# Optimization experiments

Hardware: AMD Instinct MI355X
Metric: run time of the kernel (lower is better)

## Reference

```python
import jax, jax.numpy as jnp
import numpy as np

N = 100000      # nodes
E = 1600000     # edges (avg degree 16)
F_IN = 128      # node feature dim
F_OUT = 128     # GCN output dim


def setup_inputs() -> dict:
    key = jax.random.key(0)
    ks = jax.random.split(key, 11)
    s = 0.05  # weight scale to keep activations sane
    return {
        "x": jax.random.normal(ks[0], (N, F_IN), jnp.float32),
        "edge_index": jax.random.randint(ks[1], (2, E), 0, N, jnp.int32),
        "W": jax.random.normal(ks[2], (F_IN, F_OUT), jnp.float32) * s,
        "p": jax.random.normal(ks[3], (F_IN,), jnp.float32),
        "w_ih": jax.random.normal(ks[4], (3 * F_OUT, F_IN), jnp.float32) * s,
        "w_hh": jax.random.normal(ks[5], (3 * F_OUT, F_OUT), jnp.float32) * s,
        "b_ih": jax.random.normal(ks[6], (3 * F_OUT,), jnp.float32) * s,
        "b_hh": jax.random.normal(ks[7], (3 * F_OUT,), jnp.float32) * s,
        "conv_bias": jax.random.normal(ks[8], (F_OUT,), jnp.float32) * s,
        "lin_w": jax.random.normal(ks[9], (1, F_OUT), jnp.float32) * s,
        "lin_b": jax.random.normal(ks[10], (1,), jnp.float32) * s,
    }


def reference(x, edge_index, W, p, w_ih, w_hh, b_ih, b_hh, conv_bias, lin_w, lin_b):
    n_nodes = x.shape[0]
    k, H = W.shape  # k = F_IN rows, H = F_OUT hidden size

    # --- TopK summarize: pick k nodes, gate by tanh(score) -> X_tilde [k, F_IN]
    scores = x @ p / jnp.linalg.norm(p)
    top_vals, top_idx = jax.lax.top_k(scores, k)
    x_tilde = x[top_idx] * jnp.tanh(top_vals)[:, None]

    # --- one GRU step evolving W (hidden state = rows of W)
    gi = x_tilde @ w_ih.T + b_ih   # [k, 3H]
    gh = W @ w_hh.T + b_hh         # [k, 3H]
    r = jax.nn.sigmoid(gi[:, :H] + gh[:, :H])
    z = jax.nn.sigmoid(gi[:, H:2 * H] + gh[:, H:2 * H])
    n = jnp.tanh(gi[:, 2 * H:] + r * gh[:, 2 * H:])
    W_new = (1.0 - z) * n + z * W  # [F_IN, F_OUT]

    # --- GCN conv with fixed W: sym-normalized adjacency with self loops
    row, col = edge_index[0], edge_index[1]
    deg = jax.ops.segment_sum(jnp.ones_like(row, dtype=x.dtype), col,
                              num_segments=n_nodes) + 1.0  # +1 for self loop
    dinv = jax.lax.rsqrt(deg)
    xw = x @ W_new                                   # [N, F_OUT]
    coef = dinv[row] * dinv[col]                     # [E]
    agg = jax.ops.segment_sum(xw[row] * coef[:, None], col, num_segments=n_nodes)
    agg = agg + xw * (dinv * dinv)[:, None] + conv_bias  # self-loop term + bias

    # --- head: ReLU + Linear(F_OUT, 1)
    h = jax.nn.relu(agg)
    return h @ lin_w.T + lin_b  # [N, 1]
```

## Files before the change

kernel.cpp:

```cpp
#include <hip/hip_runtime.h>
#include <math.h>

#define N_NODES 100000
#define N_EDGES 1600000
#define F 128

#define BSH 8
#define NBUCK 391
#define BCAP 5120
#define PB_EDGES 2048
#define NB_PART 782
#define NB_SCORES 1563
#define NB_COLLECT 392

typedef unsigned int u32;
typedef unsigned short u16;
typedef __attribute__((ext_vector_type(8))) short short8;
typedef __attribute__((ext_vector_type(4))) float floatx4;
typedef __attribute__((ext_vector_type(2))) float f32x2;
typedef __attribute__((ext_vector_type(4))) u32 u32x4;


__device__ __forceinline__ u32 key_of(float s) {
    u32 u = __float_as_uint(s);
    return (u & 0x80000000u) ? ~u : (u | 0x80000000u);
}

__device__ __forceinline__ float wave_reduce(float v) {
    #pragma unroll
    for (int off = 32; off > 0; off >>= 1) v += __shfl_down(v, off, 64);
    return v;
}

__device__ __forceinline__ u16 f2bf(float f) {
    u32 u = __float_as_uint(f);
    u += 0x7fffu + ((u >> 16) & 1u);
    return (u16)(u >> 16);
}

__device__ __forceinline__ float bflo(u32 b) { return __uint_as_float(b << 16); }
__device__ __forceinline__ float bfhi(u32 b) { return __uint_as_float(b & 0xffff0000u); }

__device__ __forceinline__ void pk_acc(f32x2& acc, u32 u) {
    f32x2 v; v.x = bflo(u); v.y = bfhi(u);
    asm("v_pk_add_f32 %0, %1, %0" : "+v"(acc) : "v"(v));
}
__device__ __forceinline__ void pk_add2(f32x2& a, f32x2 b) {
    asm("v_pk_add_f32 %0, %1, %0" : "+v"(a) : "v"(b));
}


__global__ void k_front(const float* __restrict__ x, const float* __restrict__ p,
                        const int* __restrict__ ei, float* __restrict__ scores,
                        u32* __restrict__ hist16, u32* __restrict__ gcur,
                        u32* __restrict__ pairs, u32* __restrict__ xb) {
    if (blockIdx.x < NB_PART) {
        __shared__ u32 lh[NBUCK];
        __shared__ u32 lbase[NBUCK];
        int t = threadIdx.x;
        int e0 = blockIdx.x * PB_EDGES;
        int e1 = e0 + PB_EDGES; if (e1 > N_EDGES) e1 = N_EDGES;
        for (int i = t; i < NBUCK; i += 256) lh[i] = 0u;
        __syncthreads();
        for (int e = e0 + t; e < e1; e += 256)
            atomicAdd(&lh[((u32)ei[N_EDGES + e]) >> BSH], 1u);
        __syncthreads();
        for (int b = t; b < NBUCK; b += 256) {
            u32 c = lh[b];
            lbase[b] = c ? atomicAdd(&gcur[b], c) : 0u;
            lh[b] = 0u;
        }
        __syncthreads();
        for (int e = e0 + t; e < e1; e += 256) {
            u32 d = (u32)ei[N_EDGES + e];
            u32 b = d >> BSH;
            u32 pos = lbase[b] + atomicAdd(&lh[b], 1u);
            pairs[(size_t)b * BCAP + pos] = ((d & 255u) << 17) | (u32)ei[e];
        }
    } else {
        int sb = blockIdx.x - NB_PART;
        int wave = threadIdx.x >> 6;
        int lane = threadIdx.x & 63;
        int q = lane >> 4, sub = lane & 15;
        int nb0 = sb * 64 + wave * 16 + q;
        float4 p0 = *(const float4*)&p[sub * 8];
        float4 p1 = *(const float4*)&p[sub * 8 + 4];
        float4 v0[4], v1[4];
        if (nb0 + 12 < N_NODES) {
            #pragma unroll
            for (int r = 0; r < 4; r++) {
                const float* xr = &x[(size_t)(nb0 + r * 4) * F + sub * 8];
                v0[r] = *(const float4*)xr;
                v1[r] = *(const float4*)(xr + 4);
            }
        } else {
            #pragma unroll
            for (int r = 0; r < 4; r++) {
                int node = nb0 + r * 4;
                v0[r] = make_float4(0.f, 0.f, 0.f, 0.f);
                v1[r] = make_float4(0.f, 0.f, 0.f, 0.f);
                if (node < N_NODES) {
                    const float* xr = &x[(size_t)node * F + sub * 8];
                    v0[r] = *(const float4*)xr;
                    v1[r] = *(const float4*)(xr + 4);
                }
            }
        }
        #pragma unroll
        for (int r = 0; r < 4; r++) {
            int node = nb0 + r * 4;
            if (node >= N_NODES) continue;
            if (xb) {
                u32x4 pk;
                pk.x = (u32)f2bf(v0[r].x) | ((u32)f2bf(v0[r].y) << 16);
                pk.y = (u32)f2bf(v0[r].z) | ((u32)f2bf(v0[r].w) << 16);
                pk.z = (u32)f2bf(v1[r].x) | ((u32)f2bf(v1[r].y) << 16);
                pk.w = (u32)f2bf(v1[r].z) | ((u32)f2bf(v1[r].w) << 16);
                *(u32x4*)&xb[(size_t)node * 64 + sub * 4] = pk;
            }
            float d = v0[r].x * p0.x + v0[r].y * p0.y + v0[r].z * p0.z + v0[r].w * p0.w
                    + v1[r].x * p1.x + v1[r].y * p1.y + v1[r].z * p1.z + v1[r].w * p1.w;
            #pragma unroll
            for (int off = 1; off < 16; off <<= 1) d += __shfl_xor(d, off, 64);
            if (sub == 0) {
                scores[node] = d;
                atomicAdd(&hist16[key_of(d) >> 16], 1u);
            }
        }
    }
}


__global__ __launch_bounds__(1024) void k_scan16(const u32* __restrict__ hist16,
                                                 u32* __restrict__ state,
                                                 const u32* __restrict__ gcur,
                                                 u32* __restrict__ bbase) {
    __shared__ u32 a[1024];
    int t = threadIdx.x;
    if (blockIdx.x == 0) {
        const uint4* h4 = (const uint4*)hist16;
        u32 local = 0;
        #pragma unroll
        for (int i = 0; i < 16; i++) {
            uint4 v = h4[t * 16 + i];
            local += v.x + v.y + v.z + v.w;
        }
        a[t] = local;
        __syncthreads();
        for (int off = 1; off < 1024; off <<= 1) {
            u32 add = (t + off < 1024) ? a[t + off] : 0u;
            __syncthreads();
            a[t] += add;
            __syncthreads();
        }
        u32 S_above = (t == 1023) ? 0u : a[t + 1];
        if (S_above < 128u && a[t] >= 128u) {
            u32 cum = S_above;
            for (int v = t * 64 + 63; v >= t * 64; v--) {
                cum += hist16[v];
                if (cum >= 128u) { state[0] = (u32)v; break; }
            }
        }
    } else {
        u32 v = (t < NBUCK) ? gcur[t] : 0u;
        a[t] = v;
        __syncthreads();
        for (int off = 1; off < 1024; off <<= 1) {
            u32 add = (t >= off) ? a[t - off] : 0u;
            __syncthreads();
            a[t] += add;
            __syncthreads();
        }
        if (t < NBUCK) bbase[t] = a[t] - v;
    }
}


__global__ __launch_bounds__(256) void k_mid(const float* __restrict__ scores,
                                             u32* __restrict__ state,
                                             u32* __restrict__ cand,
                                             const u32* __restrict__ pairs,
                                             const u32* __restrict__ gcur,
                                             const u32* __restrict__ bbase,
                                             u32* __restrict__ offs,
                                             float* __restrict__ dinv,
                                             u32* __restrict__ ebuf) {
    if (blockIdx.x < NB_COLLECT) {
        u32 T = state[0] << 16;
        int i = blockIdx.x * 256 + threadIdx.x;
        if (i < N_NODES) {
            if (key_of(scores[i]) >= T) {
                u32 pos = atomicAdd(&state[2], 1u);
                if (pos < 2048u) cand[pos] = (u32)i;
            }
        }
    } else {
        __shared__ u32 h[256];
        __shared__ u32 sc[256];
        int b = blockIdx.x - NB_COLLECT, t = threadIdx.x;
        u32 base = bbase[b];
        u32 cnt  = gcur[b];
        const u32* seg = pairs + (size_t)b * BCAP;
        u32 lo = (u32)b << BSH;
        h[t] = 0u;
        __syncthreads();
        for (u32 i = t; i < cnt; i += 256)
            atomicAdd(&h[seg[i] >> 17], 1u);
        __syncthreads();
        sc[t] = h[t];
        __syncthreads();
        for (int off = 1; off < 256; off <<= 1) {
            u32 v = (t >= off) ? sc[t - off] : 0u;
            __syncthreads();
            sc[t] += v;
            __syncthreads();
        }
        int nn = N_NODES - (int)lo;
        if (t < nn) {
            u32 c = h[t];
            offs[lo + t] = base + (sc[t] - c);
            dinv[lo + t] = rsqrtf((float)c + 1.0f);
        }
        u32 excl = sc[t] - h[t];
        __syncthreads();
        sc[t] = excl;
        __syncthreads();
        for (u32 i = t; i < cnt; i += 256) {
            u32 pr = seg[i];
            u32 pos = base + atomicAdd(&sc[pr >> 17], 1u);
            ebuf[pos] = pr & 0x1ffffu;
        }
        if (b == 0 && t == 0) offs[N_NODES] = N_EDGES;
    }
}

__global__ void k_assemble16(const float* __restrict__ scores, const float* __restrict__ p,
                             const u32* __restrict__ state, const u32* __restrict__ cand,
                             u32* __restrict__ top_idx, float* __restrict__ gate) {
    __shared__ u32 ci[2048];
    __shared__ float csc[2048];
    __shared__ float s_inv;
    int t = threadIdx.x;
    if (t < 64) {
        float2 pv = *(const float2*)&p[t * 2];
        float d = pv.x * pv.x + pv.y * pv.y;
        d = wave_reduce(d);
        if (t == 0) s_inv = rsqrtf(d);
    }
    u32 nc = state[2]; if (nc > 2048u) nc = 2048u;
    for (u32 i = t; i < nc; i += 256) { u32 ix = cand[i]; ci[i] = ix; csc[i] = scores[ix]; }
    __syncthreads();
    for (u32 i = t; i < nc; i += 256) {
        u32 myk = key_of(csc[i]);
        u32 myi = ci[i];
        int rank = 0;
        for (u32 j = 0; j < nc; j++) {
            u32 ok = key_of(csc[j]);
            rank += (int)((ok > myk) || (ok == myk && ci[j] < myi));
        }
        if (rank < 128) {
            top_idx[rank] = myi;
            gate[rank] = tanhf(csc[i] * s_inv);
        }
    }
}


__global__ __launch_bounds__(256) void k_ggemm(const float* __restrict__ x,
                                               const float* __restrict__ W,
                                               const float* __restrict__ w_ih,
                                               const float* __restrict__ w_hh,
                                               const u32* __restrict__ top_idx,
                                               const float* __restrict__ gate,
                                               float* __restrict__ G) {
    __shared__ float As[32][128];
    __shared__ float Bs[64][131];
    int t = threadIdx.x;
    int k0 = blockIdx.x * 32;
    int by = blockIdx.y;
    int j0 = by * 64;
    bool is_gi = (by < 6);
    #pragma unroll
    for (int i = 0; i < 4; i++) {
        int l = t + i * 256;
        int row = l >> 5, c4 = l & 31;
        float4 v;
        if (is_gi) {
            u32 idx = top_idx[k0 + row];
            float gt = gate[k0 + row];
            v = *(const float4*)&x[(size_t)idx * F + c4 * 4];
            v.x *= gt; v.y *= gt; v.z *= gt; v.w *= gt;
        } else {
            v = *(const float4*)&W[(k0 + row) * F + c4 * 4];
        }
        *(float4*)&As[row][c4 * 4] = v;
    }
    const float* mat = is_gi ? w_ih : w_hh;
    int jbase = is_gi ? j0 : (j0 - 384);
    #pragma unroll
    for (int i = 0; i < 8; i++) {
        int l = t + i * 256;
        int row = l >> 5, c4 = l & 31;
        float4 v = *(const float4*)&mat[(jbase + row) * F + c4 * 4];
        Bs[row][c4 * 4 + 0] = v.x; Bs[row][c4 * 4 + 1] = v.y;
        Bs[row][c4 * 4 + 2] = v.z; Bs[row][c4 * 4 + 3] = v.w;
    }
    __syncthreads();
    int ty = t >> 5, tx = t & 31;
    float acc[4][2] = {};
    #pragma unroll 4
    for (int f = 0; f < 128; f++) {
        float b0 = Bs[tx * 2][f], b1 = Bs[tx * 2 + 1][f];
        #pragma unroll
        for (int i = 0; i < 4; i++) {
            float a = As[ty * 4 + i][f];
            acc[i][0] += a * b0;
            acc[i][1] += a * b1;
        }
    }
    #pragma unroll
    for (int i = 0; i < 4; i++) {
        int k = k0 + ty * 4 + i;
        G[(size_t)k * 768 + j0 + tx * 2 + 0] = acc[i][0];
        G[(size_t)k * 768 + j0 + tx * 2 + 1] = acc[i][1];
    }
}


__global__ void k_gate(const float* __restrict__ G, const float* __restrict__ W,
                       const float* __restrict__ b_ih, const float* __restrict__ b_hh,
                       float* __restrict__ Wnew, u16* __restrict__ Bfrag) {
    int idx = blockIdx.x * blockDim.x + threadIdx.x;
    int k = idx >> 7, h = idx & 127;
    const float* gk = &G[(size_t)k * 768];
    float gir = gk[h]       + b_ih[h];
    float giz = gk[128 + h] + b_ih[128 + h];
    float gin = gk[256 + h] + b_ih[256 + h];
    float ghr = gk[384 + h] + b_hh[h];
    float ghz = gk[512 + h] + b_hh[128 + h];
    float ghn = gk[640 + h] + b_hh[256 + h];
    float wv  = W[k * F + h];
    float rg = 1.0f / (1.0f + expf(-(gir + ghr)));
    float z  = 1.0f / (1.0f + expf(-(giz + ghz)));
    float n  = tanhf(gin + rg * ghn);
    float val = (1.0f - z) * n + z * wv;
    Wnew[k * F + h] = val;
    int nb = h >> 4, kc = k >> 5, q = (k >> 3) & 3, m = h & 15, jj = k & 7;
    Bfrag[(((nb * 4 + kc) * 64) + q * 16 + m) * 8 + jj] = f2bf(val);
}


__device__ __forceinline__ void gemm_core(u16* As, const u16* __restrict__ Bfrag,
                                          const float* __restrict__ dinv,
                                          u16* __restrict__ yw, int r0, int t) {
    int wv = t >> 6, lane = t & 63;
    int q = lane >> 4, m = lane & 15;
    floatx4 acc[8] = {};
    #pragma unroll
    for (int kc = 0; kc < 4; kc++) {
        short8 a = *(const short8*)&As[((wv * 4 + kc) * 64 + lane) * 8];
        #pragma unroll
        for (int nb = 0; nb < 8; nb++) {
            short8 bfr = *(const short8*)&Bfrag[((nb * 4 + kc) * 64 + lane) * 8];
            acc[nb] = __builtin_amdgcn_mfma_f32_16x16x32_bf16(a, bfr, acc[nb], 0, 0, 0);
        }
    }
    __syncthreads();

    float d[4];
    #pragma unroll
    for (int reg = 0; reg < 4; reg++) {
        int gr = r0 + wv * 16 + q * 4 + reg;
        d[reg] = (gr < N_NODES) ? dinv[gr] : 0.f;
    }
    #pragma unroll
    for (int nb = 0; nb < 8; nb++) {
        #pragma unroll
        for (int reg = 0; reg < 4; reg++) {
            int row = wv * 16 + q * 4 + reg;
            As[row * 132 + nb * 16 + m] = f2bf(acc[nb][reg] * d[reg]);
        }
    }
    __syncthreads();
    {
        int row = t >> 2, segi = t & 3;
        int gr = r0 + row;
        if (gr < N_NODES) {
            const uint2* src = (const uint2*)&As[row * 132 + segi * 32];
            uint2* dst = (uint2*)&yw[(size_t)gr * F + segi * 32];
            #pragma unroll
            for (int i = 0; i < 8; i++) dst[i] = src[i];
        }
    }
}

__global__ __launch_bounds__(256) void k_gemm(const float* __restrict__ x,
                                              const u16* __restrict__ Bfrag,
                                              const float* __restrict__ dinv,
                                              u16* __restrict__ yw) {
    __shared__ __align__(16) u16 As[8448];
    int t = threadIdx.x;
    int r0 = blockIdx.x * 64;
    #pragma unroll
    for (int i = 0; i < 8; i++) {
        int l = t + i * 256;
        int row = l >> 5, c4 = l & 31;
        int f0 = c4 * 4;
        float4 v = {0.f, 0.f, 0.f, 0.f};
        if (r0 + row < N_NODES) v = *(const float4*)&x[(size_t)(r0 + row) * F + f0];
        int widx = (((row >> 4) * 4 + (f0 >> 5)) * 64 + ((f0 >> 3) & 3) * 16 + (row & 15)) * 8
                   + (f0 & 7);
        ushort4 s4;
        s4.x = f2bf(v.x); s4.y = f2bf(v.y); s4.z = f2bf(v.z); s4.w = f2bf(v.w);
        *(ushort4*)&As[widx] = s4;
    }
    __syncthreads();
    gemm_core(As, Bfrag, dinv, yw, r0, t);
}

__global__ __launch_bounds__(256) void k_gemm_xb(const u32* __restrict__ xb,
                                                 const u16* __restrict__ Bfrag,
                                                 const float* __restrict__ dinv,
                                                 u16* __restrict__ yw) {
    __shared__ __align__(16) u16 As[8448];
    int t = threadIdx.x;
    int r0 = blockIdx.x * 64;
    #pragma unroll
    for (int i = 0; i < 4; i++) {
        int wdx = t + i * 256;
        int lane = wdx & 63, chunk = wdx >> 6;
        int kc = chunk & 3, rowhi = chunk >> 2;
        int q = lane >> 4, m = lane & 15;
        int row = rowhi * 16 + m;
        u32x4 v = {0u, 0u, 0u, 0u};
        if (r0 + row < N_NODES)
            v = *(const u32x4*)&xb[(size_t)(r0 + row) * 64 + kc * 16 + q * 4];
        *(u32x4*)&As[wdx * 8] = v;
    }
    __syncthreads();
    gemm_core(As, Bfrag, dinv, yw, r0, t);
}


#define EDGE_GROUP(J) {                                                      \
    u32 r = ebuf[(J) + q];                                                   \
    uint4 bb = *(const uint4*)&yw32[(size_t)r * 64 + sub * 4];               \
    pk_acc(a01, bb.x); pk_acc(a23, bb.y);                                    \
    pk_acc(a45, bb.z); pk_acc(a67, bb.w); }

#define BFLY(A) {                                                            \
    f32x2 tb;                                                                \
    tb.x = __shfl_xor(A.x, 16, 64); tb.y = __shfl_xor(A.y, 16, 64);          \
    pk_add2(A, tb);                                                          \
    tb.x = __shfl_xor(A.x, 32, 64); tb.y = __shfl_xor(A.y, 32, 64);          \
    pk_add2(A, tb); }

__global__ void k_gather(const u32* __restrict__ yw32, const u32* __restrict__ offs,
                         const u32* __restrict__ ebuf, const float* __restrict__ dinv,
                         const float* __restrict__ conv_bias, const float* __restrict__ lin_w,
                         const float* __restrict__ lin_b, float* __restrict__ out,
                         int node0) {
    int c = node0 + blockIdx.x * 4 + (threadIdx.x >> 6);
    if (c >= N_NODES) return;
    int lane = threadIdx.x & 63;
    int q = lane >> 4, sub = lane & 15;
    u32 jbeg = offs[c], jend = offs[c + 1];
    f32x2 a01 = {0.f, 0.f}, a23 = {0.f, 0.f}, a45 = {0.f, 0.f}, a67 = {0.f, 0.f};
    u32 j = jbeg;
    for (; j + 16 <= jend; j += 16) {
        EDGE_GROUP(j) EDGE_GROUP(j + 4) EDGE_GROUP(j + 8) EDGE_GROUP(j + 12)
    }
    for (; j + 4 <= jend; j += 4) EDGE_GROUP(j)
    u32 rem = jend - j;
    if (rem) {
        u32 idx = ((u32)q < rem) ? (j + q) : j;
        u32 r = ebuf[idx];
        uint4 bb = *(const uint4*)&yw32[(size_t)r * 64 + sub * 4];
        if ((u32)q < rem) {
            pk_acc(a01, bb.x); pk_acc(a23, bb.y);
            pk_acc(a45, bb.z); pk_acc(a67, bb.w);
        }
    }
    BFLY(a01) BFLY(a23) BFLY(a45) BFLY(a67)
    float dc = dinv[c];
    uint4 sb = *(const uint4*)&yw32[(size_t)c * 64 + sub * 4];
    float4 cb0 = *(const float4*)&conv_bias[sub * 8];
    float4 cb1 = *(const float4*)&conv_bias[sub * 8 + 4];
    float4 lw0 = *(const float4*)&lin_w[sub * 8];
    float4 lw1 = *(const float4*)&lin_w[sub * 8 + 4];
    float h0 = fmaxf(dc * (a01.x + bflo(sb.x)) + cb0.x, 0.f);
    float h1 = fmaxf(dc * (a01.y + bfhi(sb.x)) + cb0.y, 0.f);
    float h2 = fmaxf(dc * (a23.x + bflo(sb.y)) + cb0.z, 0.f);
    float h3 = fmaxf(dc * (a23.y + bfhi(sb.y)) + cb0.w, 0.f);
    float h4 = fmaxf(dc * (a45.x + bflo(sb.z)) + cb1.x, 0.f);
    float h5 = fmaxf(dc * (a45.y + bfhi(sb.z)) + cb1.y, 0.f);
    float h6 = fmaxf(dc * (a67.x + bflo(sb.w)) + cb1.z, 0.f);
    float h7 = fmaxf(dc * (a67.y + bfhi(sb.w)) + cb1.w, 0.f);
    float part = (h0 * lw0.x + h1 * lw0.y + h2 * lw0.z + h3 * lw0.w)
               + (h4 * lw1.x + h5 * lw1.y + h6 * lw1.z + h7 * lw1.w);
    #pragma unroll
    for (int off = 8; off > 0; off >>= 1) part += __shfl_down(part, off, 64);
    if (lane == 0) out[c] = part + lin_b[0];
}


extern "C" void kernel_launch(void* const* d_in, const int* in_sizes, int n_in,
                              void* d_out, int out_size, void* d_ws, size_t ws_size,
                              hipStream_t stream) {
    const float* x         = (const float*)d_in[0];
    const int*   ei        = (const int*)  d_in[1];
    const float* W         = (const float*)d_in[2];
    const float* p         = (const float*)d_in[3];
    const float* w_ih      = (const float*)d_in[4];
    const float* w_hh      = (const float*)d_in[5];
    const float* b_ih      = (const float*)d_in[6];
    const float* b_hh      = (const float*)d_in[7];
    const float* conv_bias = (const float*)d_in[8];
    const float* lin_w     = (const float*)d_in[9];
    const float* lin_b     = (const float*)d_in[10];
    float* out = (float*)d_out;

    u32*   w  = (u32*)d_ws;
    float* wf = (float*)d_ws;

    const size_t SCORES_W = 0;
    const size_t DINV_W   = 100096;
    const size_t OFFS_W   = 200192;
    const size_t HIST16_W = 300288;
    const size_t STATE_W  = 365824;
    const size_t GCUR_W   = 365832;
    const size_t BBASE_W  = 366224;
    const size_t CAND_W   = 366616;
    const size_t TOPI_W   = 368664;
    const size_t GATE_W   = 368792;
    const size_t WNEW_W   = 368920;
    const size_t BFRAG_W  = 385304;
    const size_t PAIRS_W  = 389400;
    const size_t EBUF_W   = 2400000;
    const size_t YW_W     = 4000000;
    const size_t XB_W     = 10400000;

    float* scores  = wf + SCORES_W;
    float* dinv    = wf + DINV_W;
    u32*   offs    = w  + OFFS_W;
    u32*   hist16  = w  + HIST16_W;
    u32*   state   = w  + STATE_W;
    u32*   gcur    = w  + GCUR_W;
    u32*   bbase   = w  + BBASE_W;
    u32*   cand    = w  + CAND_W;
    u32*   top_idx = w  + TOPI_W;
    float* gate    = wf + GATE_W;
    float* Wnew    = wf + WNEW_W;
    u16*   Bfrag   = (u16*)(w + BFRAG_W);
    u32*   pairs   = w  + PAIRS_W;
    float* G       = wf + PAIRS_W;
    u32*   ebuf    = w  + EBUF_W;
    u16*   yw      = (u16*)(w + YW_W);
    u32*   yw32    = w + YW_W;

    bool   use_xb  = ws_size >= (XB_W + 6400000) * sizeof(u32);
    u32*   xb      = use_xb ? (w + XB_W) : (u32*)0;

    hipMemsetAsync(hist16, 0, (65536 + 8 + NBUCK) * sizeof(u32), stream);

    k_front<<<NB_PART + NB_SCORES, 256, 0, stream>>>(x, p, ei, scores, hist16,
                                                     gcur, pairs, xb);
    k_scan16<<<2, 1024, 0, stream>>>(hist16, state, gcur, bbase);
    k_mid<<<NB_COLLECT + NBUCK, 256, 0, stream>>>(scores, state, cand, pairs, gcur,
                                                  bbase, offs, dinv, ebuf);
    k_assemble16<<<1, 256, 0, stream>>>(scores, p, state, cand, top_idx, gate);

    k_ggemm<<<dim3(4, 12), 256, 0, stream>>>(x, W, w_ih, w_hh, top_idx, gate, G);
    k_gate<<<64, 256, 0, stream>>>(G, W, b_ih, b_hh, Wnew, Bfrag);

    if (use_xb) k_gemm_xb<<<1563, 256, 0, stream>>>(xb, Bfrag, dinv, yw);
    else        k_gemm   <<<1563, 256, 0, stream>>>(x,  Bfrag, dinv, yw);

    k_gather<<<12500, 256, 0, stream>>>(yw32, offs, ebuf, dinv, conv_bias, lin_w,
                                        lin_b, out, 0);
    k_gather<<<12500, 256, 0, stream>>>(yw32, offs, ebuf, dinv, conv_bias, lin_w,
                                        lin_b, out, 50000);
}
```

Before: 301.4 us.

## Split front kernel, fuse top-k assembly into GRU GEMM, split gather launches

Splits the combined partition/score kernel into two separate launches. Folds the single-block top-k rank assembly into every k_ggemm block, so each block recomputes the ranks and keeps indices and gates in shared memory, removing one launch and a global round trip. Also splits the gather into four smaller launches instead of two. This trades a serial single-block launch for redundant rank work across 48 blocks, and adds extra launches elsewhere.

```diff
diff --git a/kernel.cpp b/kernel.cpp
--- a/kernel.cpp
+++ b/kernel.cpp
@@ -50,82 +50,86 @@
 }
 
 
-__global__ void k_front(const float* __restrict__ x, const float* __restrict__ p,
-                        const int* __restrict__ ei, float* __restrict__ scores,
-                        u32* __restrict__ hist16, u32* __restrict__ gcur,
-                        u32* __restrict__ pairs, u32* __restrict__ xb) {
-    if (blockIdx.x < NB_PART) {
-        __shared__ u32 lh[NBUCK];
-        __shared__ u32 lbase[NBUCK];
-        int t = threadIdx.x;
-        int e0 = blockIdx.x * PB_EDGES;
-        int e1 = e0 + PB_EDGES; if (e1 > N_EDGES) e1 = N_EDGES;
-        for (int i = t; i < NBUCK; i += 256) lh[i] = 0u;
-        __syncthreads();
-        for (int e = e0 + t; e < e1; e += 256)
-            atomicAdd(&lh[((u32)ei[N_EDGES + e]) >> BSH], 1u);
-        __syncthreads();
-        for (int b = t; b < NBUCK; b += 256) {
-            u32 c = lh[b];
-            lbase[b] = c ? atomicAdd(&gcur[b], c) : 0u;
-            lh[b] = 0u;
-        }
-        __syncthreads();
-        for (int e = e0 + t; e < e1; e += 256) {
-            u32 d = (u32)ei[N_EDGES + e];
-            u32 b = d >> BSH;
-            u32 pos = lbase[b] + atomicAdd(&lh[b], 1u);
-            pairs[(size_t)b * BCAP + pos] = ((d & 255u) << 17) | (u32)ei[e];
+__global__ __launch_bounds__(256) void k_part(const int* __restrict__ ei,
+                                              u32* __restrict__ gcur,
+                                              u32* __restrict__ pairs) {
+    __shared__ u32 lh[NBUCK];
+    __shared__ u32 lbase[NBUCK];
+    int t = threadIdx.x;
+    int e0 = blockIdx.x * PB_EDGES;
+    int e1 = e0 + PB_EDGES; if (e1 > N_EDGES) e1 = N_EDGES;
+    for (int i = t; i < NBUCK; i += 256) lh[i] = 0u;
+    __syncthreads();
+    for (int e = e0 + t; e < e1; e += 256)
+        atomicAdd(&lh[((u32)ei[N_EDGES + e]) >> BSH], 1u);
+    __syncthreads();
+    for (int b = t; b < NBUCK; b += 256) {
+        u32 c = lh[b];
+        lbase[b] = c ? atomicAdd(&gcur[b], c) : 0u;
+        lh[b] = 0u;
+    }
+    __syncthreads();
+    for (int e = e0 + t; e < e1; e += 256) {
+        u32 d = (u32)ei[N_EDGES + e];
+        u32 b = d >> BSH;
+        u32 pos = lbase[b] + atomicAdd(&lh[b], 1u);
+        pairs[(size_t)b * BCAP + pos] = ((d & 255u) << 17) | (u32)ei[e];
+    }
+}
+
+
+__global__ __launch_bounds__(256) void k_scores(const float* __restrict__ x,
+                                                const float* __restrict__ p,
+                                                float* __restrict__ scores,
+                                                u32* __restrict__ hist16,
+                                                u32* __restrict__ xb) {
+    int sb = blockIdx.x;
+    int wave = threadIdx.x >> 6;
+    int lane = threadIdx.x & 63;
+    int q = lane >> 4, sub = lane & 15;
+    int nb0 = sb * 64 + wave * 16 + q;
+    float4 p0 = *(const float4*)&p[sub * 8];
+    float4 p1 = *(const float4*)&p[sub * 8 + 4];
+    float4 v0[4], v1[4];
+    if (nb0 + 12 < N_NODES) {
+        #pragma unroll
+        for (int r = 0; r < 4; r++) {
+            const float* xr = &x[(size_t)(nb0 + r * 4) * F + sub * 8];
+            v0[r] = *(const float4*)xr;
+            v1[r] = *(const float4*)(xr + 4);
         }
     } else {
-        int sb = blockIdx.x - NB_PART;
-        int wave = threadIdx.x >> 6;
-        int lane = threadIdx.x & 63;
-        int q = lane >> 4, sub = lane & 15;
-        int nb0 = sb * 64 + wave * 16 + q;
-        float4 p0 = *(const float4*)&p[sub * 8];
-        float4 p1 = *(const float4*)&p[sub * 8 + 4];
-        float4 v0[4], v1[4];
-        if (nb0 + 12 < N_NODES) {
-            #pragma unroll
-            for (int r = 0; r < 4; r++) {
-                const float* xr = &x[(size_t)(nb0 + r * 4) * F + sub * 8];
+        #pragma unroll
+        for (int r = 0; r < 4; r++) {
+            int node = nb0 + r * 4;
+            v0[r] = make_float4(0.f, 0.f, 0.f, 0.f);
+            v1[r] = make_float4(0.f, 0.f, 0.f, 0.f);
+            if (node < N_NODES) {
+                const float* xr = &x[(size_t)node * F + sub * 8];
                 v0[r] = *(const float4*)xr;
                 v1[r] = *(const float4*)(xr + 4);
             }
-        } else {
-            #pragma unroll
-            for (int r = 0; r < 4; r++) {
-                int node = nb0 + r * 4;
-                v0[r] = make_float4(0.f, 0.f, 0.f, 0.f);
-                v1[r] = make_float4(0.f, 0.f, 0.f, 0.f);
-                if (node < N_NODES) {
-                    const float* xr = &x[(size_t)node * F + sub * 8];
-                    v0[r] = *(const float4*)xr;
-                    v1[r] = *(const float4*)(xr + 4);
-                }
-            }
-        }
-        #pragma unroll
-        for (int r = 0; r < 4; r++) {
-            int node = nb0 + r * 4;
-            if (node >= N_NODES) continue;
-            if (xb) {
-                u32x4 pk;
-                pk.x = (u32)f2bf(v0[r].x) | ((u32)f2bf(v0[r].y) << 16);
-                pk.y = (u32)f2bf(v0[r].z) | ((u32)f2bf(v0[r].w) << 16);
-                pk.z = (u32)f2bf(v1[r].x) | ((u32)f2bf(v1[r].y) << 16);
-                pk.w = (u32)f2bf(v1[r].z) | ((u32)f2bf(v1[r].w) << 16);
-                *(u32x4*)&xb[(size_t)node * 64 + sub * 4] = pk;
-            }
-            float d = v0[r].x * p0.x + v0[r].y * p0.y + v0[r].z * p0.z + v0[r].w * p0.w
-                    + v1[r].x * p1.x + v1[r].y * p1.y + v1[r].z * p1.z + v1[r].w * p1.w;
-            #pragma unroll
-            for (int off = 1; off < 16; off <<= 1) d += __shfl_xor(d, off, 64);
-            if (sub == 0) {
-                scores[node] = d;
-                atomicAdd(&hist16[key_of(d) >> 16], 1u);
-            }
+        }
+    }
+    #pragma unroll
+    for (int r = 0; r < 4; r++) {
+        int node = nb0 + r * 4;
+        if (node >= N_NODES) continue;
+        if (xb) {
+            u32x4 pk;
+            pk.x = (u32)f2bf(v0[r].x) | ((u32)f2bf(v0[r].y) << 16);
+            pk.y = (u32)f2bf(v0[r].z) | ((u32)f2bf(v0[r].w) << 16);
+            pk.z = (u32)f2bf(v1[r].x) | ((u32)f2bf(v1[r].y) << 16);
+            pk.w = (u32)f2bf(v1[r].z) | ((u32)f2bf(v1[r].w) << 16);
+            *(u32x4*)&xb[(size_t)node * 64 + sub * 4] = pk;
+        }
+        float d = v0[r].x * p0.x + v0[r].y * p0.y + v0[r].z * p0.z + v0[r].w * p0.w
+                + v1[r].x * p1.x + v1[r].y * p1.y + v1[r].z * p1.z + v1[r].w * p1.w;
+        #pragma unroll
+        for (int off = 1; off < 16; off <<= 1) d += __shfl_xor(d, off, 64);
+        if (sub == 0) {
+            scores[node] = d;
+            atomicAdd(&hist16[key_of(d) >> 16], 1u);
         }
     }
 }
@@ -234,13 +238,24 @@
     }
 }
 
-__global__ void k_assemble16(const float* __restrict__ scores, const float* __restrict__ p,
-                             const u32* __restrict__ state, const u32* __restrict__ cand,
-                             u32* __restrict__ top_idx, float* __restrict__ gate) {
-    __shared__ u32 ci[2048];
-    __shared__ float csc[2048];
+
+__global__ __launch_bounds__(256) void k_ggemm(const float* __restrict__ x,
+                                               const float* __restrict__ W,
+                                               const float* __restrict__ w_ih,
+                                               const float* __restrict__ w_hh,
+                                               const float* __restrict__ scores,
+                                               const float* __restrict__ p,
+                                               const u32* __restrict__ state,
+                                               const u32* __restrict__ cand,
+                                               float* __restrict__ G) {
+    __shared__ float As[32][128];
+    __shared__ float Bs[64][131];
+    __shared__ u32 s_topi[128];
+    __shared__ float s_gate[128];
     __shared__ float s_inv;
     int t = threadIdx.x;
+    u32*   ci  = (u32*)&Bs[0][0];
+    float* csc = (float*)&Bs[16][0];
     if (t < 64) {
         float2 pv = *(const float2*)&p[t * 2];
         float d = pv.x * pv.x + pv.y * pv.y;
@@ -259,23 +274,12 @@
             rank += (int)((ok > myk) || (ok == myk && ci[j] < myi));
         }
         if (rank < 128) {
-            top_idx[rank] = myi;
-            gate[rank] = tanhf(csc[i] * s_inv);
-        }
-    }
-}
-
-
-__global__ __launch_bounds__(256) void k_ggemm(const float* __restrict__ x,
-                                               const float* __restrict__ W,
-                                               const float* __restrict__ w_ih,
-                                               const float* __restrict__ w_hh,
-                                               const u32* __restrict__ top_idx,
-                                               const float* __restrict__ gate,
-                                               float* __restrict__ G) {
-    __shared__ float As[32][128];
-    __shared__ float Bs[64][131];
-    int t = threadIdx.x;
+            s_topi[rank] = myi;
+            s_gate[rank] = tanhf(csc[i] * s_inv);
+        }
+    }
+    __syncthreads();
+
     int k0 = blockIdx.x * 32;
     int by = blockIdx.y;
     int j0 = by * 64;
@@ -286,8 +290,8 @@
         int row = l >> 5, c4 = l & 31;
         float4 v;
         if (is_gi) {
-            u32 idx = top_idx[k0 + row];
-            float gt = gate[k0 + row];
+            u32 idx = s_topi[k0 + row];
+            float gt = s_gate[k0 + row];
             v = *(const float4*)&x[(size_t)idx * F + c4 * 4];
             v.x *= gt; v.y *= gt; v.z *= gt; v.w *= gt;
         } else {
@@ -531,8 +535,6 @@
     const size_t GCUR_W   = 365832;
     const size_t BBASE_W  = 366224;
     const size_t CAND_W   = 366616;
-    const size_t TOPI_W   = 368664;
-    const size_t GATE_W   = 368792;
     const size_t WNEW_W   = 368920;
     const size_t BFRAG_W  = 385304;
     const size_t PAIRS_W  = 389400;
@@ -548,8 +550,6 @@
     u32*   gcur    = w  + GCUR_W;
     u32*   bbase   = w  + BBASE_W;
     u32*   cand    = w  + CAND_W;
-    u32*   top_idx = w  + TOPI_W;
-    float* gate    = wf + GATE_W;
     float* Wnew    = wf + WNEW_W;
     u16*   Bfrag   = (u16*)(w + BFRAG_W);
     u32*   pairs   = w  + PAIRS_W;
@@ -563,21 +563,24 @@
 
     hipMemsetAsync(hist16, 0, (65536 + 8 + NBUCK) * sizeof(u32), stream);
 
-    k_front<<<NB_PART + NB_SCORES, 256, 0, stream>>>(x, p, ei, scores, hist16,
-                                                     gcur, pairs, xb);
+    k_part<<<NB_PART, 256, 0, stream>>>(ei, gcur, pairs);
+    k_scores<<<NB_SCORES, 256, 0, stream>>>(x, p, scores, hist16, xb);
     k_scan16<<<2, 1024, 0, stream>>>(hist16, state, gcur, bbase);
     k_mid<<<NB_COLLECT + NBUCK, 256, 0, stream>>>(scores, state, cand, pairs, gcur,
                                                   bbase, offs, dinv, ebuf);
-    k_assemble16<<<1, 256, 0, stream>>>(scores, p, state, cand, top_idx, gate);
-
-    k_ggemm<<<dim3(4, 12), 256, 0, stream>>>(x, W, w_ih, w_hh, top_idx, gate, G);
+    k_ggemm<<<dim3(4, 12), 256, 0, stream>>>(x, W, w_ih, w_hh, scores, p, state,
+                                             cand, G);
     k_gate<<<64, 256, 0, stream>>>(G, W, b_ih, b_hh, Wnew, Bfrag);
 
     if (use_xb) k_gemm_xb<<<1563, 256, 0, stream>>>(xb, Bfrag, dinv, yw);
     else        k_gemm   <<<1563, 256, 0, stream>>>(x,  Bfrag, dinv, yw);
 
-    k_gather<<<12500, 256, 0, stream>>>(yw32, offs, ebuf, dinv, conv_bias, lin_w,
-                                        lin_b, out, 0);
-    k_gather<<<12500, 256, 0, stream>>>(yw32, offs, ebuf, dinv, conv_bias, lin_w,
-                                        lin_b, out, 50000);
-}
+    k_gather<<<6250, 256, 0, stream>>>(yw32, offs, ebuf, dinv, conv_bias, lin_w,
+                                       lin_b, out, 0);
+    k_gather<<<6250, 256, 0, stream>>>(yw32, offs, ebuf, dinv, conv_bias, lin_w,
+                                       lin_b, out, 25000);
+    k_gather<<<6250, 256, 0, stream>>>(yw32, offs, ebuf, dinv, conv_bias, lin_w,
+                                       lin_b, out, 50000);
+    k_gather<<<6250, 256, 0, stream>>>(yw32, offs, ebuf, dinv, conv_bias, lin_w,
+                                       lin_b, out, 75000);
+}
```

New measurement: 346.1 us. +14.8%, slower.
